# Performance work log

Measured on AMD Instinct MI355X. Metric: run time of the kernel, lower is better.

## Reference

```python
import jax, jax.numpy as jnp
import numpy as np

EMBED_DIM = 256
NUM_HEADS = 8
HEAD_DIM = EMBED_DIM // NUM_HEADS
NUM_POINTS_LIST = [4, 4, 4, 4]
PT = sum(NUM_POINTS_LIST)  # 16 points per head, total_points = 8*16 = 128
OFFSET_SCALE = 0.5
SHAPES = np.array([[128, 128], [64, 64], [32, 32], [16, 16]], dtype=np.int32)
BS, LQ = 8, 1000


def setup_inputs() -> dict:
    key = jax.random.key(0)
    ks = jax.random.split(key, 12)
    Lv = int((SHAPES[:, 0] * SHAPES[:, 1]).sum())  # 21760
    C = EMBED_DIM
    s = 0.02
    return {
        "query": jax.random.normal(ks[0], (BS, LQ, C), jnp.float32),
        "reference_points": jax.random.uniform(ks[1], (BS, LQ, 1, 4), jnp.float32, 0.1, 0.9),
        "value": jax.random.normal(ks[2], (BS, Lv, C), jnp.float32),
        "spatial_shapes": SHAPES,  # static numpy, not traced
        "w_off": jax.random.normal(ks[3], (C, NUM_HEADS * PT * 2), jnp.float32) * s,
        "b_off": jax.random.normal(ks[4], (NUM_HEADS * PT * 2,), jnp.float32) * 0.5,
        "w_attn": jax.random.normal(ks[5], (C, NUM_HEADS * PT), jnp.float32) * s,
        "b_attn": jnp.zeros((NUM_HEADS * PT,), jnp.float32),
        "w_val": jax.random.normal(ks[6], (C, C), jnp.float32) * s,
        "b_val": jnp.zeros((C,), jnp.float32),
        "w_out": jax.random.normal(ks[7], (C, C), jnp.float32) * s,
        "b_out": jnp.zeros((C,), jnp.float32),
    }


def _sample_level(v, loc, H, W):
    """Bilinear sample (grid_sample, align_corners=False, zero padding).
    v:   [bs, nH, H*W, hd]  value features of one pyramid level
    loc: [bs, Lq, nH, P, 2] sampling locations in [0,1] (x, y)
    returns [bs, Lq, nH, P, hd]
    """
    bs, Lq, nH, P, _ = loc.shape
    hd = v.shape[-1]
    x = loc[..., 0] * W - 0.5
    y = loc[..., 1] * H - 0.5
    x0 = jnp.floor(x)
    y0 = jnp.floor(y)
    lx = x - x0
    ly = y - y0
    x0i = x0.astype(jnp.int32)
    y0i = y0.astype(jnp.int32)

    def corner(xi, yi, w):
        valid = (xi >= 0) & (xi < W) & (yi >= 0) & (yi < H)
        idx = jnp.clip(yi, 0, H - 1) * W + jnp.clip(xi, 0, W - 1)  # [bs,Lq,nH,P]
        idxf = jnp.transpose(idx, (0, 2, 1, 3)).reshape(bs, nH, Lq * P)
        g = jnp.take_along_axis(v, idxf[..., None], axis=2)  # [bs,nH,Lq*P,hd]
        wv = jnp.where(valid, w, 0.0).astype(v.dtype)
        wf = jnp.transpose(wv, (0, 2, 1, 3)).reshape(bs, nH, Lq * P, 1)
        return g * wf

    out = (corner(x0i, y0i, (1 - lx) * (1 - ly))
           + corner(x0i + 1, y0i, lx * (1 - ly))
           + corner(x0i, y0i + 1, (1 - lx) * ly)
           + corner(x0i + 1, y0i + 1, lx * ly))
    out = out.reshape(bs, nH, Lq, P, hd)
    return jnp.transpose(out, (0, 2, 1, 3, 4))


def reference(query, reference_points, value, spatial_shapes,
              w_off, b_off, w_attn, b_attn, w_val, b_val, w_out, b_out):
    shapes = np.asarray(spatial_shapes)  # static
    bs, Lq, C = query.shape
    Lv = value.shape[1]
    nH, hd, Pt = NUM_HEADS, HEAD_DIM, PT

    # value projection -> [bs, nH, Lv, hd]
    v = value @ w_val + b_val
    v = jnp.transpose(v.reshape(bs, Lv, nH, hd), (0, 2, 1, 3))

    # sampling offsets and attention weights from query
    off = (query @ w_off + b_off).reshape(bs, Lq, nH, Pt, 2)
    aw = jax.nn.softmax((query @ w_attn + b_attn).reshape(bs, Lq, nH, Pt), axis=-1)

    # reference_points: [bs, Lq, 1, 4] boxes (cx, cy, w, h) in [0,1]
    nps = jnp.asarray([1.0 / n for n in NUM_POINTS_LIST for _ in range(n)],
                      dtype=query.dtype)[:, None]  # [Pt,1]
    loc = (reference_points[:, :, None, :, :2]
           + off * nps * reference_points[:, :, None, :, 2:] * OFFSET_SCALE)  # [bs,Lq,nH,Pt,2]

    samples = []
    v_start = 0
    p_start = 0
    for l, (H, W) in enumerate(shapes):
        H, W = int(H), int(W)
        P = NUM_POINTS_LIST[l]
        v_l = jax.lax.dynamic_slice_in_dim(v, v_start, H * W, axis=2)
        loc_l = loc[:, :, :, p_start:p_start + P, :]
        samples.append(_sample_level(v_l, loc_l, H, W))
        v_start += H * W
        p_start += P
    samples = jnp.concatenate(samples, axis=3)  # [bs,Lq,nH,Pt,hd]

    out = jnp.einsum('blhp,blhpd->blhd', aw, samples).reshape(bs, Lq, C)
    return out @ w_out + b_out
```

## Files before the change

kernel.cpp:

```cpp
#include <hip/hip_runtime.h>

typedef unsigned short ushort_t;
typedef short s16x8 __attribute__((ext_vector_type(8)));
typedef float f32x4 __attribute__((ext_vector_type(4)));
typedef unsigned short u16x4 __attribute__((ext_vector_type(4)));
typedef unsigned int uint2_t __attribute__((ext_vector_type(2)));
typedef unsigned int uint4_t __attribute__((ext_vector_type(4)));

#define KDIM 256
#define BK 64
#define LDST 72
#define LV_TOTAL 21760
#define NQ 8000
#define VM_TILES2 680
#define QOA_BLOCKS 96
#define VPROJ_BLOCKS 672

__device__ inline unsigned short f2b(float f) {
  union { float f; unsigned u; } v; v.f = f;
  return (unsigned short)((v.u + 0x7fffu + ((v.u >> 16) & 1u)) >> 16);
}
__device__ inline float b2f(unsigned short h) {
  union { unsigned u; float f; } v; v.u = ((unsigned)h) << 16;
  return v.f;
}
__device__ inline unsigned pack_bf16x2(float lo, float hi) {
  union { float f; unsigned u; } a, b;
  a.f = lo; b.f = hi;
  return __builtin_amdgcn_perm(b.u + 0x8000u, a.u + 0x8000u, 0x07060302u);
}
__device__ inline unsigned short f2b_cheap(float f) {
  union { float f; unsigned u; } v; v.f = f;
  return (unsigned short)((v.u + 0x8000u) >> 16);
}

__global__ __launch_bounds__(256) void prep_weights(
    const float* __restrict__ w_off, const float* __restrict__ w_attn,
    const float* __restrict__ w_val, const float* __restrict__ w_out,
    const float* __restrict__ b_off, const float* __restrict__ b_attn,
    ushort_t* __restrict__ wt_val, ushort_t* __restrict__ wt_qoa,
    ushort_t* __restrict__ wt_out, float* __restrict__ bias_qoa,
    int* __restrict__ counters)
{
  int bid = blockIdx.x;
  int k = threadIdx.x;
  if (bid < 256) {
    int n = bid;
    wt_val[n*KDIM + k] = f2b(w_val[k*256 + n]);
  } else if (bid < 640) {
    int n = bid - 256;
    float v = (n < 256) ? w_off[k*256 + n] : w_attn[k*128 + (n - 256)];
    wt_qoa[n*KDIM + k] = f2b(v);
  } else if (bid < 896) {
    int n = bid - 640;
    wt_out[n*KDIM + k] = f2b(w_out[k*256 + n]);
  } else {
    if (k < 2) counters[k] = 0;
    for (int i = k; i < 384; i += 256)
      bias_qoa[i] = (i < 256) ? b_off[i] : b_attn[i - 256];
  }
}

__global__ __launch_bounds__(512) void merged_gemms(
    const float* __restrict__ value, const ushort_t* __restrict__ wt_val,
    const float* __restrict__ b_val, ushort_t* __restrict__ v_proj,
    const float* __restrict__ query, const ushort_t* __restrict__ wt_qoa,
    const float* __restrict__ bias_qoa, float* __restrict__ qoa,
    int* __restrict__ counters)
{
  __shared__ __align__(16) char smem[65536];
  __shared__ int s_mt;
  const int tid  = threadIdx.x;
  const int wave = tid >> 6;
  const int lane = tid & 63;
  const int lrow = lane & 15;
  const int quad = lane >> 4;

  if (blockIdx.x < QOA_BLOCKS) {
    ushort_t* sA = (ushort_t*)smem;
    ushort_t* sB = (ushort_t*)(smem + 256 * LDST * 2);
    const int m0 = (blockIdx.x % 32) * 256;
    const int n0 = (blockIdx.x / 32) * 128;
    const int M = NQ, N = 384;

    f32x4 acc[2][8];
    #pragma unroll
    for (int i = 0; i < 2; ++i)
      #pragma unroll
      for (int j = 0; j < 8; ++j) acc[i][j] = {0.f, 0.f, 0.f, 0.f};

    for (int kc = 0; kc < KDIM; kc += BK) {
      #pragma unroll
      for (int i = 0; i < 8; ++i) {
        int f   = tid + i * 512;
        int row = f >> 4;
        int c4  = f & 15;
        int gr  = m0 + row;
        float4 val = {0.f, 0.f, 0.f, 0.f};
        if (gr < M) val = *(const float4*)(query + (size_t)gr * KDIM + kc + c4 * 4);
        uint2_t t;
        t.x = pack_bf16x2(val.x, val.y);
        t.y = pack_bf16x2(val.z, val.w);
        *(uint2_t*)&sA[row * LDST + c4 * 4] = t;
      }
      #pragma unroll
      for (int i = 0; i < 2; ++i) {
        int f   = tid + i * 512;
        int row = f >> 3;
        int seg = f & 7;
        s16x8 v = *(const s16x8*)(wt_qoa + (size_t)(n0 + row) * KDIM + kc + seg * 8);
        *(s16x8*)&sB[row * LDST + seg * 8] = v;
      }
      __syncthreads();
      #pragma unroll
      for (int ki = 0; ki < BK; ki += 32) {
        int krow = ki + quad * 8;
        s16x8 af[2], bfr[8];
        #pragma unroll
        for (int mt = 0; mt < 2; ++mt)
          af[mt] = *(const s16x8*)&sA[(wave * 32 + mt * 16 + lrow) * LDST + krow];
        #pragma unroll
        for (int nt = 0; nt < 8; ++nt)
          bfr[nt] = *(const s16x8*)&sB[(nt * 16 + lrow) * LDST + krow];
        #pragma unroll
        for (int mt = 0; mt < 2; ++mt)
          #pragma unroll
          for (int nt = 0; nt < 8; ++nt)
            acc[mt][nt] = __builtin_amdgcn_mfma_f32_16x16x32_bf16(
                af[mt], bfr[nt], acc[mt][nt], 0, 0, 0);
      }
      __syncthreads();
    }
    #pragma unroll
    for (int mt = 0; mt < 2; ++mt) {
      int gmb = m0 + wave * 32 + mt * 16 + quad * 4;
      #pragma unroll
      for (int nt = 0; nt < 8; ++nt) {
        int gn = n0 + nt * 16 + lrow;
        float bvv = bias_qoa[gn];
        #pragma unroll
        for (int r = 0; r < 4; ++r) {
          int gm = gmb + r;
          if (gm < M) qoa[(size_t)gm * N + gn] = acc[mt][nt][r] + bvv;
        }
      }
    }
    return;
  }

  ushort_t* sB = (ushort_t*)smem;
  const int vbid = blockIdx.x - QOA_BLOCKS;
  const int half = vbid & 1;
  const int n0   = half * 128;

  {
    const ushort_t* src = wt_val + (size_t)n0 * KDIM;
    #pragma unroll
    for (int i = 0; i < 8; ++i) {
      int g   = tid + i * 512;
      int row = g >> 5;
      int c   = g & 31;
      s16x8 v = *(const s16x8*)(src + row * KDIM + c * 8);
      *(s16x8*)&sB[row * 256 + ((c ^ (row & 7)) * 8)] = v;
    }
  }
  __syncthreads();

  float bv[8];
  #pragma unroll
  for (int nt = 0; nt < 8; ++nt) bv[nt] = b_val[n0 + nt * 16 + lrow];

  const int swz = lrow & 7;

  while (true) {
    if (tid == 0) s_mt = atomicAdd(&counters[half], 1);
    __syncthreads();
    const int mt = s_mt;
    if (mt >= VM_TILES2) break;
    const int m0 = mt * 256;
    const float* arow0 = value + (size_t)(m0 + wave * 32 + lrow) * KDIM + quad * 8;
    const float* arow1 = arow0 + 16 * KDIM;

    f32x4 acc[2][8];
    #pragma unroll
    for (int m = 0; m < 2; ++m)
      #pragma unroll
      for (int nt = 0; nt < 8; ++nt) acc[m][nt] = {0.f, 0.f, 0.f, 0.f};

    float4 st[2][2][2];
    st[0][0][0] = *(const float4*)(arow0);
    st[0][0][1] = *(const float4*)(arow0 + 4);
    st[0][1][0] = *(const float4*)(arow1);
    st[0][1][1] = *(const float4*)(arow1 + 4);

    #pragma unroll
    for (int ks = 0; ks < 8; ++ks) {
      const int cur = ks & 1, nxt = cur ^ 1;
      if (ks < 7) {
        const float* p0 = arow0 + (ks + 1) * 32;
        const float* p1 = arow1 + (ks + 1) * 32;
        st[nxt][0][0] = *(const float4*)(p0);
        st[nxt][0][1] = *(const float4*)(p0 + 4);
        st[nxt][1][0] = *(const float4*)(p1);
        st[nxt][1][1] = *(const float4*)(p1 + 4);
      }
      s16x8 af[2];
      #pragma unroll
      for (int m = 0; m < 2; ++m) {
        union { uint4_t d; s16x8 v; } u;
        u.d.x = pack_bf16x2(st[cur][m][0].x, st[cur][m][0].y);
        u.d.y = pack_bf16x2(st[cur][m][0].z, st[cur][m][0].w);
        u.d.z = pack_bf16x2(st[cur][m][1].x, st[cur][m][1].y);
        u.d.w = pack_bf16x2(st[cur][m][1].z, st[cur][m][1].w);
        af[m] = u.v;
      }
      #pragma unroll
      for (int nt = 0; nt < 8; ++nt) {
        s16x8 bf = *(const s16x8*)&sB[(nt * 16 + lrow) * 256 +
                                      (((4 * ks + quad) ^ swz) * 8)];
        acc[0][nt] = __builtin_amdgcn_mfma_f32_16x16x32_bf16(af[0], bf, acc[0][nt], 0, 0, 0);
        acc[1][nt] = __builtin_amdgcn_mfma_f32_16x16x32_bf16(af[1], bf, acc[1][nt], 0, 0, 0);
      }
    }

    #pragma unroll
    for (int m = 0; m < 2; ++m) {
      int gm = m0 + wave * 32 + m * 16 + quad * 4;
      #pragma unroll
      for (int nt = 0; nt < 8; ++nt) {
        int gn = n0 + nt * 16 + lrow;
        #pragma unroll
        for (int r = 0; r < 4; ++r)
          v_proj[(size_t)(gm + r) * KDIM + gn] = f2b_cheap(acc[m][nt][r] + bv[nt]);
      }
    }
    __syncthreads();
  }
}

__global__ __launch_bounds__(256) void ms_deform_sample(
    const ushort_t* __restrict__ v,
    const float* __restrict__ qoa,
    const float* __restrict__ refp,
    float* __restrict__ outq)
{
  __shared__ float s_w[512];
  __shared__ int   s_i[512];
  const int bq  = blockIdx.x;
  const int b   = bq / 1000;
  const int tid = threadIdx.x;

  if (tid < 128) {
    const int p = tid & 15;
    const float* qrow = qoa + (size_t)bq * 384;
    float logit = qrow[256 + tid];
    float mx = logit;
    #pragma unroll
    for (int s = 8; s >= 1; s >>= 1) mx = fmaxf(mx, __shfl_xor(mx, s, 16));
    float e = __expf(logit - mx);
    float sum = e;
    #pragma unroll
    for (int s = 8; s >= 1; s >>= 1) sum += __shfl_xor(sum, s, 16);
    float aw = e / sum;

    float ox = qrow[tid * 2], oy = qrow[tid * 2 + 1];
    const float* rp = refp + (size_t)bq * 4;
    float rx = rp[0], ry = rp[1], rw = rp[2], rh = rp[3];
    const int lvl = p >> 2;
    const int HWs[4] = {128, 64, 32, 16};
    const int STs[4] = {0, 16384, 20480, 21504};
    int W = HWs[lvl], H = HWs[lvl], st = STs[lvl];
    float lx = rx + ox * 0.125f * rw;
    float ly = ry + oy * 0.125f * rh;
    float x = lx * (float)W - 0.5f;
    float y = ly * (float)H - 0.5f;
    float x0f = floorf(x), y0f = floorf(y);
    int x0 = (int)x0f, y0 = (int)y0f;
    float fx = x - x0f, fy = y - y0f;
    float wc[4] = {(1.f - fx) * (1.f - fy), fx * (1.f - fy),
                   (1.f - fx) * fy,         fx * fy};
    #pragma unroll
    for (int c = 0; c < 4; ++c) {
      int xi = x0 + (c & 1);
      int yi = y0 + (c >> 1);
      bool valid = (xi >= 0) && (xi < W) && (yi >= 0) && (yi < H);
      int xc = min(max(xi, 0), W - 1);
      int yc = min(max(yi, 0), H - 1);
      s_w[tid * 4 + c] = valid ? wc[c] * aw : 0.f;
      s_i[tid * 4 + c] = st + yc * W + xc;
    }
  }
  __syncthreads();

  const int h   = tid >> 5;
  const int l32 = tid & 31;
  const int grp = l32 >> 2;
  const int sub = l32 & 3;
  const ushort_t* vb = v + (size_t)b * LV_TOTAL * 256 + h * 32 + sub * 8;

  float wreg[8]; int ireg[8];
  #pragma unroll
  for (int i = 0; i < 8; ++i) {
    int j = h * 64 + i * 8 + grp;
    wreg[i] = s_w[j];
    ireg[i] = s_i[j];
  }
  s16x8 vv[8];
  #pragma unroll
  for (int i = 0; i < 8; ++i)
    vv[i] = *(const s16x8*)(vb + (size_t)ireg[i] * 256);

  float acc[8];
  #pragma unroll
  for (int d = 0; d < 8; ++d) acc[d] = 0.f;
  #pragma unroll
  for (int i = 0; i < 8; ++i)
    #pragma unroll
    for (int d = 0; d < 8; ++d)
      acc[d] += wreg[i] * b2f((ushort_t)vv[i][d]);

  #pragma unroll
  for (int m = 4; m <= 16; m <<= 1)
    #pragma unroll
    for (int d = 0; d < 8; ++d)
      acc[d] += __shfl_xor(acc[d], m);

  if (l32 < 4) {
    float* dst = outq + (size_t)bq * 256 + h * 32 + l32 * 8;
    float4 o0 = {acc[0], acc[1], acc[2], acc[3]};
    float4 o1 = {acc[4], acc[5], acc[6], acc[7]};
    *(float4*)dst = o0;
    *(float4*)(dst + 4) = o1;
  }
}

__global__ __launch_bounds__(256) void gemm_bf16(
    const float* __restrict__ A, const ushort_t* __restrict__ Bt,
    const float* __restrict__ bias, float* __restrict__ Cf,
    int M, int N)
{
  __shared__ ushort_t sA[128 * LDST];
  __shared__ ushort_t sB[64 * LDST];
  const int tid  = threadIdx.x;
  const int m0   = blockIdx.x * 128;
  const int n0   = blockIdx.y * 64;
  const int wave = tid >> 6;
  const int lane = tid & 63;
  const int lrow = lane & 15;
  const int quad = lane >> 4;

  f32x4 acc[2][4];
  #pragma unroll
  for (int i = 0; i < 2; ++i)
    #pragma unroll
    for (int j = 0; j < 4; ++j) acc[i][j] = {0.f, 0.f, 0.f, 0.f};

  for (int kc = 0; kc < KDIM; kc += BK) {
    #pragma unroll
    for (int i = 0; i < 8; ++i) {
      int f   = tid + i * 256;
      int row = f >> 4;
      int c4  = f & 15;
      int gr  = m0 + row;
      float4 val = {0.f, 0.f, 0.f, 0.f};
      if (gr < M) val = *(const float4*)(A + (size_t)gr * KDIM + kc + c4 * 4);
      uint2_t t;
      t.x = pack_bf16x2(val.x, val.y);
      t.y = pack_bf16x2(val.z, val.w);
      *(uint2_t*)&sA[row * LDST + c4 * 4] = t;
    }
    #pragma unroll
    for (int i = 0; i < 2; ++i) {
      int f   = tid + i * 256;
      int row = f >> 3;
      int seg = f & 7;
      s16x8 v = *(const s16x8*)(Bt + (size_t)(n0 + row) * KDIM + kc + seg * 8);
      *(s16x8*)&sB[row * LDST + seg * 8] = v;
    }
    __syncthreads();
    #pragma unroll
    for (int ki = 0; ki < BK; ki += 32) {
      int krow = ki + quad * 8;
      s16x8 af[2], bfr[4];
      #pragma unroll
      for (int mt = 0; mt < 2; ++mt)
        af[mt] = *(const s16x8*)&sA[(wave * 32 + mt * 16 + lrow) * LDST + krow];
      #pragma unroll
      for (int nt = 0; nt < 4; ++nt)
        bfr[nt] = *(const s16x8*)&sB[(nt * 16 + lrow) * LDST + krow];
      #pragma unroll
      for (int mt = 0; mt < 2; ++mt)
        #pragma unroll
        for (int nt = 0; nt < 4; ++nt)
          acc[mt][nt] = __builtin_amdgcn_mfma_f32_16x16x32_bf16(
              af[mt], bfr[nt], acc[mt][nt], 0, 0, 0);
    }
    __syncthreads();
  }
  #pragma unroll
  for (int mt = 0; mt < 2; ++mt) {
    int gmb = m0 + wave * 32 + mt * 16 + quad * 4;
    #pragma unroll
    for (int nt = 0; nt < 4; ++nt) {
      int gn = n0 + nt * 16 + lrow;
      float bvv = bias[gn];
      #pragma unroll
      for (int r = 0; r < 4; ++r) {
        int gm = gmb + r;
        if (gm < M) Cf[(size_t)gm * N + gn] = acc[mt][nt][r] + bvv;
      }
    }
  }
}

extern "C" void kernel_launch(void* const* d_in, const int* in_sizes, int n_in,
                              void* d_out, int out_size, void* d_ws, size_t ws_size,
                              hipStream_t stream) {
  const float* query  = (const float*)d_in[0];
  const float* refp   = (const float*)d_in[1];
  const float* value  = (const float*)d_in[2];
  const float* w_off  = (const float*)d_in[4];
  const float* b_off  = (const float*)d_in[5];
  const float* w_attn = (const float*)d_in[6];
  const float* b_attn = (const float*)d_in[7];
  const float* w_val  = (const float*)d_in[8];
  const float* b_val  = (const float*)d_in[9];
  const float* w_out  = (const float*)d_in[10];
  const float* b_out  = (const float*)d_in[11];
  float* out = (float*)d_out;

  char* ws = (char*)d_ws;
  const size_t WS_NEEDED = 110069760;
  if (ws_size < WS_NEEDED) return;
  ushort_t* wt_val   = (ushort_t*)(ws);
  ushort_t* wt_qoa   = (ushort_t*)(ws + 131072);
  ushort_t* wt_out   = (ushort_t*)(ws + 327680);
  float*    bias_qoa = (float*)   (ws + 458752);
  int*      counters = (int*)     (ws + 460288);
  ushort_t* v_proj   = (ushort_t*)(ws + 460800);
  float*    qoa      = (float*)   (ws + 89589760);
  float*    outq     = (float*)   (ws + 101877760);

  prep_weights<<<897, 256, 0, stream>>>(w_off, w_attn, w_val, w_out, b_off, b_attn,
                                        wt_val, wt_qoa, wt_out, bias_qoa, counters);
  merged_gemms<<<QOA_BLOCKS + VPROJ_BLOCKS, 512, 0, stream>>>(
      value, wt_val, b_val, v_proj, query, wt_qoa, bias_qoa, qoa, counters);
  ms_deform_sample<<<NQ, 256, 0, stream>>>(v_proj, qoa, refp, outq);
  gemm_bf16<<<dim3(63, 4), 256, 0, stream>>>(outq, wt_out, b_out, out, NQ, 256);
}
```

Measured before the change: 357.3 us.

## Switch value projection to per-wave strip scheduling with cross-tile prefetch

The value-projection GEMM now hands out work per wave in 32-row strips through a wave-level atomic counter, instead of per block in 256-row tiles. This removes the block-wide barriers and the shared-memory broadcast of the tile index. The A-operand register prefetch grows from double to quad buffering, and it loads the first k-slices of the next strip while the current strip finishes, so global loads overlap the tail of compute. The VPROJ block count also drops. The costs are more atomics and higher register use from the larger staging buffers.

```diff
diff --git a/kernel.cpp b/kernel.cpp
--- a/kernel.cpp
+++ b/kernel.cpp
@@ -12,9 +12,9 @@
 #define LDST 72
 #define LV_TOTAL 21760
 #define NQ 8000
-#define VM_TILES2 680
+#define NSTRIPS 5440
 #define QOA_BLOCKS 96
-#define VPROJ_BLOCKS 672
+#define VPROJ_BLOCKS 512
 
 __device__ inline unsigned short f2b(float f) {
   union { float f; unsigned u; } v; v.f = f;
@@ -69,7 +69,6 @@
     int* __restrict__ counters)
 {
   __shared__ __align__(16) char smem[65536];
-  __shared__ int s_mt;
   const int tid  = threadIdx.x;
   const int wave = tid >> 6;
   const int lane = tid & 63;
@@ -172,46 +171,52 @@
 
   const int swz = lrow & 7;
 
-  while (true) {
-    if (tid == 0) s_mt = atomicAdd(&counters[half], 1);
-    __syncthreads();
-    const int mt = s_mt;
-    if (mt >= VM_TILES2) break;
-    const int m0 = mt * 256;
-    const float* arow0 = value + (size_t)(m0 + wave * 32 + lrow) * KDIM + quad * 8;
-    const float* arow1 = arow0 + 16 * KDIM;
-
+  float4 st[4][2][2];
+
+#define LOADK(BUF, MM0, KK) do {                                              \
+    const float* _p = value + (size_t)((MM0) + lrow) * KDIM + (KK) * 32 + quad * 8; \
+    st[BUF][0][0] = *(const float4*)(_p);                                     \
+    st[BUF][0][1] = *(const float4*)(_p + 4);                                 \
+    st[BUF][1][0] = *(const float4*)(_p + 16 * KDIM);                         \
+    st[BUF][1][1] = *(const float4*)(_p + 16 * KDIM + 4);                     \
+  } while (0)
+
+  int s;
+  {
+    int t = 0;
+    if (lane == 0) t = atomicAdd(&counters[half], 1);
+    s = __builtin_amdgcn_readfirstlane(t);
+  }
+  if (s < NSTRIPS) { LOADK(0, s * 32, 0); LOADK(1, s * 32, 1); }
+
+  while (s < NSTRIPS) {
+    int tnext = 0;
+    if (lane == 0) tnext = atomicAdd(&counters[half], 1);
+
+    const int m0 = s * 32;
     f32x4 acc[2][8];
     #pragma unroll
     for (int m = 0; m < 2; ++m)
       #pragma unroll
       for (int nt = 0; nt < 8; ++nt) acc[m][nt] = {0.f, 0.f, 0.f, 0.f};
 
-    float4 st[2][2][2];
-    st[0][0][0] = *(const float4*)(arow0);
-    st[0][0][1] = *(const float4*)(arow0 + 4);
-    st[0][1][0] = *(const float4*)(arow1);
-    st[0][1][1] = *(const float4*)(arow1 + 4);
-
+    int snext = 0;
     #pragma unroll
     for (int ks = 0; ks < 8; ++ks) {
-      const int cur = ks & 1, nxt = cur ^ 1;
-      if (ks < 7) {
-        const float* p0 = arow0 + (ks + 1) * 32;
-        const float* p1 = arow1 + (ks + 1) * 32;
-        st[nxt][0][0] = *(const float4*)(p0);
-        st[nxt][0][1] = *(const float4*)(p0 + 4);
-        st[nxt][1][0] = *(const float4*)(p1);
-        st[nxt][1][1] = *(const float4*)(p1 + 4);
+      if (ks == 6) snext = __builtin_amdgcn_readfirstlane(tnext);
+      if (ks < 6) {
+        LOADK((ks + 2) & 3, m0, ks + 2);
+      } else if (snext < NSTRIPS) {
+        LOADK((ks + 2) & 3, snext * 32, ks - 6);
       }
       s16x8 af[2];
       #pragma unroll
       for (int m = 0; m < 2; ++m) {
         union { uint4_t d; s16x8 v; } u;
-        u.d.x = pack_bf16x2(st[cur][m][0].x, st[cur][m][0].y);
-        u.d.y = pack_bf16x2(st[cur][m][0].z, st[cur][m][0].w);
-        u.d.z = pack_bf16x2(st[cur][m][1].x, st[cur][m][1].y);
-        u.d.w = pack_bf16x2(st[cur][m][1].z, st[cur][m][1].w);
+        u.d.x = pack_bf16x2(st[ks & 3][m][0].x, st[ks & 3][m][0].y);
+        u.d.y = pack_bf16x2(st[ks & 3][m][0].z, st[ks & 3][m][0].w);
+        u.d.z = pack_bf16x2(st[ks & 3][m][1].x, st[ks & 3][m][1].y);
+        u.d.w = pack_bf16x2(st[ks & 3][m][1].z, st[ks & 3][m][1].w);
         af[m] = u.v;
       }
       #pragma unroll
@@ -225,7 +230,7 @@
 
     #pragma unroll
     for (int m = 0; m < 2; ++m) {
-      int gm = m0 + wave * 32 + m * 16 + quad * 4;
+      int gm = m0 + m * 16 + quad * 4;
       #pragma unroll
       for (int nt = 0; nt < 8; ++nt) {
         int gn = n0 + nt * 16 + lrow;
@@ -234,8 +239,9 @@
           v_proj[(size_t)(gm + r) * KDIM + gn] = f2b_cheap(acc[m][nt][r] + bv[nt]);
       }
     }
-    __syncthreads();
-  }
+    s = snext;
+  }
+#undef LOADK
 }
 
 __global__ __launch_bounds__(256) void ms_deform_sample(
```

New measurement: 490.1 us. 1.37x slower.

## Store projected values head-major and vectorize GEMM epilogues via swapped MFMA operands

Applied to the files above, without the earlier changes.

The value projection now writes its bf16 output as [batch*head][Lv][32] rather than [batch][Lv][256], so each bilinear corner gather in the sampling kernel reads a compact 64-byte head slice with better locality. The QOA and output GEMMs swap their MFMA A/B operands so each lane holds four consecutive columns, which lets the epilogue use float4 bias loads and float4 stores. The two work-stealing counters are moved 64 ints apart to avoid sharing a cache line. The head-major write in the value GEMM becomes scattered 2-byte stores at a 64-byte stride, which may cost write efficiency.

```diff
diff --git a/kernel.cpp b/kernel.cpp
--- a/kernel.cpp
+++ b/kernel.cpp
@@ -3,7 +3,6 @@
 typedef unsigned short ushort_t;
 typedef short s16x8 __attribute__((ext_vector_type(8)));
 typedef float f32x4 __attribute__((ext_vector_type(4)));
-typedef unsigned short u16x4 __attribute__((ext_vector_type(4)));
 typedef unsigned int uint2_t __attribute__((ext_vector_type(2)));
 typedef unsigned int uint4_t __attribute__((ext_vector_type(4)));
 
@@ -11,6 +10,7 @@
 #define BK 64
 #define LDST 72
 #define LV_TOTAL 21760
+#define HL 696320
 #define NQ 8000
 #define VM_TILES2 680
 #define QOA_BLOCKS 96
@@ -55,7 +55,7 @@
     int n = bid - 640;
     wt_out[n*KDIM + k] = f2b(w_out[k*256 + n]);
   } else {
-    if (k < 2) counters[k] = 0;
+    if (k < 128) counters[k] = 0;
     for (int i = k; i < 384; i += 256)
       bias_qoa[i] = (i < 256) ? b_off[i] : b_attn[i - 256];
   }
@@ -127,21 +127,21 @@
           #pragma unroll
           for (int nt = 0; nt < 8; ++nt)
             acc[mt][nt] = __builtin_amdgcn_mfma_f32_16x16x32_bf16(
-                af[mt], bfr[nt], acc[mt][nt], 0, 0, 0);
+                bfr[nt], af[mt], acc[mt][nt], 0, 0, 0);
       }
       __syncthreads();
     }
     #pragma unroll
     for (int mt = 0; mt < 2; ++mt) {
-      int gmb = m0 + wave * 32 + mt * 16 + quad * 4;
-      #pragma unroll
-      for (int nt = 0; nt < 8; ++nt) {
-        int gn = n0 + nt * 16 + lrow;
-        float bvv = bias_qoa[gn];
-        #pragma unroll
-        for (int r = 0; r < 4; ++r) {
-          int gm = gmb + r;
-          if (gm < M) qoa[(size_t)gm * N + gn] = acc[mt][nt][r] + bvv;
+      const int gm = m0 + wave * 32 + mt * 16 + lrow;
+      if (gm < M) {
+        #pragma unroll
+        for (int nt = 0; nt < 8; ++nt) {
+          const int gn = n0 + nt * 16 + quad * 4;
+          const float4 b4 = *(const float4*)(bias_qoa + gn);
+          float4 o = {acc[mt][nt][0] + b4.x, acc[mt][nt][1] + b4.y,
+                      acc[mt][nt][2] + b4.z, acc[mt][nt][3] + b4.w};
+          *(float4*)(qoa + (size_t)gm * N + gn) = o;
         }
       }
     }
@@ -173,11 +173,13 @@
   const int swz = lrow & 7;
 
   while (true) {
-    if (tid == 0) s_mt = atomicAdd(&counters[half], 1);
+    if (tid == 0) s_mt = atomicAdd(&counters[half * 64], 1);
     __syncthreads();
     const int mt = s_mt;
     if (mt >= VM_TILES2) break;
     const int m0 = mt * 256;
+    const int bidx  = mt / 85;
+    const int rbase = m0 - bidx * 21760;
     const float* arow0 = value + (size_t)(m0 + wave * 32 + lrow) * KDIM + quad * 8;
     const float* arow1 = arow0 + 16 * KDIM;
 
@@ -225,13 +227,16 @@
 
     #pragma unroll
     for (int m = 0; m < 2; ++m) {
-      int gm = m0 + wave * 32 + m * 16 + quad * 4;
+      int rl = rbase + wave * 32 + m * 16 + quad * 4;
       #pragma unroll
       for (int nt = 0; nt < 8; ++nt) {
         int gn = n0 + nt * 16 + lrow;
+        int h  = gn >> 5;
+        int d  = gn & 31;
+        ushort_t* dst = v_proj + (size_t)(bidx * 8 + h) * HL + (size_t)rl * 32 + d;
         #pragma unroll
         for (int r = 0; r < 4; ++r)
-          v_proj[(size_t)(gm + r) * KDIM + gn] = f2b_cheap(acc[m][nt][r] + bv[nt]);
+          dst[r * 32] = f2b_cheap(acc[m][nt][r] + bv[nt]);
       }
     }
     __syncthreads();
@@ -296,7 +301,7 @@
   const int l32 = tid & 31;
   const int grp = l32 >> 2;
   const int sub = l32 & 3;
-  const ushort_t* vb = v + (size_t)b * LV_TOTAL * 256 + h * 32 + sub * 8;
+  const ushort_t* vb = v + (size_t)(b * 8 + h) * HL + sub * 8;
 
   float wreg[8]; int ireg[8];
   #pragma unroll
@@ -308,7 +313,7 @@
   s16x8 vv[8];
   #pragma unroll
   for (int i = 0; i < 8; ++i)
-    vv[i] = *(const s16x8*)(vb + (size_t)ireg[i] * 256);
+    vv[i] = *(const s16x8*)(vb + (size_t)ireg[i] * 32);
 
   float acc[8];
   #pragma unroll
@@ -393,21 +398,21 @@
         #pragma unroll
         for (int nt = 0; nt < 4; ++nt)
           acc[mt][nt] = __builtin_amdgcn_mfma_f32_16x16x32_bf16(
-              af[mt], bfr[nt], acc[mt][nt], 0, 0, 0);
+              bfr[nt], af[mt], acc[mt][nt], 0, 0, 0);
     }
     __syncthreads();
   }
   #pragma unroll
   for (int mt = 0; mt < 2; ++mt) {
-    int gmb = m0 + wave * 32 + mt * 16 + quad * 4;
-    #pragma unroll
-    for (int nt = 0; nt < 4; ++nt) {
-      int gn = n0 + nt * 16 + lrow;
-      float bvv = bias[gn];
-      #pragma unroll
-      for (int r = 0; r < 4; ++r) {
-        int gm = gmb + r;
-        if (gm < M) Cf[(size_t)gm * N + gn] = acc[mt][nt][r] + bvv;
+    const int gm = m0 + wave * 32 + mt * 16 + lrow;
+    if (gm < M) {
+      #pragma unroll
+      for (int nt = 0; nt < 4; ++nt) {
+        const int gn = n0 + nt * 16 + quad * 4;
+        const float4 b4 = *(const float4*)(bias + gn);
+        float4 o = {acc[mt][nt][0] + b4.x, acc[mt][nt][1] + b4.y,
+                    acc[mt][nt][2] + b4.z, acc[mt][nt][3] + b4.w};
+        *(float4*)(Cf + (size_t)gm * N + gn) = o;
       }
     }
   }
```

Measured after the change: 352.3 us. About the same (-1.4%).
